# Kernel tuning notes

Hardware: AMD Instinct MI355X
Metric: run time of the kernel (lower is better)

Reference implementation:

```python
import jax, jax.numpy as jnp
import numpy as np

LOG2 = 0.6931471805599453
GAMMA = 10.0
NUM_KERNELS = 301
N_LAYERS = 3


def ssp(v):
    # ShiftedSoftplus: softplus(x) - log(2)
    return jax.nn.softplus(v) - jnp.asarray(LOG2, v.dtype)


def setup_inputs() -> dict:
    key = jax.random.key(0)
    ks = jax.random.split(key, 20)
    N, F, K, L, V = 512, 128, NUM_KERNELS, N_LAYERS, 100
    s = 0.05
    return {
        "x": jax.random.randint(ks[0], (N,), 0, V),
        "r": jax.random.uniform(ks[1], (N, 3), dtype=jnp.float32) * 10.0,
        "emb": jax.random.normal(ks[2], (V, F), dtype=jnp.float32),
        "aw_W": jax.random.normal(ks[3], (L, F, F), dtype=jnp.float32) * s,
        "aw_b": jax.random.normal(ks[4], (L, F), dtype=jnp.float32) * s,
        "cf_W1": jax.random.normal(ks[5], (L, K, F), dtype=jnp.float32) * s,
        "cf_b1": jax.random.normal(ks[6], (L, F), dtype=jnp.float32) * s,
        "cf_W2": jax.random.normal(ks[7], (L, F, F), dtype=jnp.float32) * s,
        "cf_b2": jax.random.normal(ks[8], (L, F), dtype=jnp.float32) * s,
        "n_W1": jax.random.normal(ks[9], (L, F, F), dtype=jnp.float32) * s,
        "n_b1": jax.random.normal(ks[10], (L, F), dtype=jnp.float32) * s,
        "n_W2": jax.random.normal(ks[11], (L, F, F), dtype=jnp.float32) * s,
        "n_b2": jax.random.normal(ks[12], (L, F), dtype=jnp.float32) * s,
        "out_W1": jax.random.normal(ks[13], (F, 32), dtype=jnp.float32) * s,
        "out_b1": jax.random.normal(ks[14], (32,), dtype=jnp.float32) * s,
        "out_W2": jax.random.normal(ks[15], (32, 1), dtype=jnp.float32) * s,
        "out_b2": jax.random.normal(ks[16], (1,), dtype=jnp.float32) * s,
    }


def reference(x, r, emb, aw_W, aw_b, cf_W1, cf_b1, cf_W2, cf_b2,
              n_W1, n_b1, n_W2, n_b2, out_W1, out_b1, out_W2, out_b2):
    centers = jnp.linspace(0.0, 30.0, NUM_KERNELS, dtype=r.dtype)  # [K]
    # pairwise distances (torch.cdist, p=2) with safe sqrt at the diagonal
    diff = r[:, None, :] - r[None, :, :]                 # [N,N,3]
    d2 = jnp.sum(diff * diff, axis=-1)                   # [N,N]
    mask = d2 > 0
    d = jnp.where(mask, jnp.sqrt(jnp.where(mask, d2, 1.0)), 0.0)

    h = emb[x]                                           # [N,F]
    for l in range(N_LAYERS):
        o = h @ aw_W[l] + aw_b[l]                        # atom-wise linear
        # Gaussian RBF expansion: [N,N,K]
        e = jnp.exp(-GAMMA * jnp.square(d[..., None] - centers))
        # filter-generating MLP: [N,N,F]
        w = ssp(e @ cf_W1[l] + cf_b1[l])
        w = ssp(w @ cf_W2[l] + cf_b2[l])
        # continuous-filter conv: o[i,k] = sum_j x[j,k] * w[i,j,k]
        c = jnp.einsum('jk,ijk->ik', o, w)
        c = ssp(c @ n_W1[l] + n_b1[l]) @ n_W2[l] + n_b2[l]
        h = h + c
    out = ssp(h @ out_W1 + out_b1) @ out_W2 + out_b2     # [N,1]
    # AdaptiveAvgPool1d(1) on a 2D [N,1] tensor is identity over L=1
    return out.reshape(-1)
```

## Files before the change

### kernel.cpp

```cpp
#include <hip/hip_runtime.h>
#include <hip/hip_fp16.h>
#include <math.h>

#define N_ATOMS 512
#define F_DIM   128
#define K_RBF   301
#define NLAYER  3
#define GAMMA_C 10.0f
#define LOG2_C  0.6931471805599453f

#define TAB_H     0.01f
#define TAB_INVH  100.0f
#define TAB_ROWS  1768
#define RPB       8
#define ROW_BYTES 512

__device__ __forceinline__ float ssp(float x) {
    float ax = fabsf(x);
    return fmaxf(x, 0.0f) + log1pf(expf(-ax)) - LOG2_C;
}
__device__ __forceinline__ __half2 u2h2(unsigned u) {
    union { unsigned u; __half2 h; } c; c.u = u; return c.h;
}
__device__ __forceinline__ unsigned h22u(__half2 h) {
    union { unsigned u; __half2 h; } c; c.h = h; return c.u;
}

__global__ void prep_kernel(const int* __restrict__ x, const float* __restrict__ r,
                            const float* __restrict__ emb,
                            const float* __restrict__ aw_W, const float* __restrict__ aw_b,
                            uint2* __restrict__ dpk, float* __restrict__ h,
                            unsigned* __restrict__ opk) {
    int i = blockIdx.x;
    int t = threadIdx.x;
    __shared__ float hs[F_DIM];
    __shared__ float os[F_DIM];
    float rx = r[i * 3 + 0], ry = r[i * 3 + 1], rz = r[i * 3 + 2];
    if (t < F_DIM) {
        float hv = emb[x[i] * F_DIM + t];
        h[i * F_DIM + t] = hv;
        hs[t] = hv;
    }
    for (int j = t; j < N_ATOMS; j += 256) {
        float dx = rx - r[j * 3 + 0];
        float dy = ry - r[j * 3 + 1];
        float dz = rz - r[j * 3 + 2];
        float d  = sqrtf(dx * dx + dy * dy + dz * dz);
        float xb = d * TAB_INVH;
        int   b  = ::min((int)xb, TAB_ROWS - 2);
        float fr = xb - (float)b;
        __half fh = __float2half(fr);
        dpk[i * N_ATOMS + j] = make_uint2((unsigned)b * ROW_BYTES,
                                          h22u(__halves2half2(fh, fh)));
    }
    __syncthreads();
    if (t < F_DIM) {
        float acc = aw_b[t];
        for (int g = 0; g < F_DIM; ++g) acc = fmaf(hs[g], aw_W[g * F_DIM + t], acc);
        os[t] = acc;
    }
    __syncthreads();
    if (t < F_DIM / 2)
        opk[i * 64 + t] = h22u(__halves2half2(__float2half(os[2 * t]),
                                              __float2half(os[2 * t + 1])));
}

__global__ void build_tables(const float* __restrict__ cf_W1, const float* __restrict__ cf_b1,
                             const float* __restrict__ cf_W2, const float* __restrict__ cf_b2,
                             uint2* __restrict__ ptab) {
    int row0 = blockIdx.x * RPB;
    int l    = blockIdx.y;
    int f    = threadIdx.x;

    float dlo = row0 * TAB_H;
    float dhi = (row0 + RPB) * TAB_H;
    int k0 = ::max(0, (int)ceilf((dlo - 1.45f) * 10.0f));
    int k1 = ::min(K_RBF - 1, (int)floorf((dhi + 1.45f) * 10.0f));
    int kw = k1 - k0 + 1;

    __shared__ float e_s[RPB + 1][34];
    __shared__ float w1_s[F_DIM][12];
    __shared__ float outs[RPB + 1][F_DIM];

    for (int idx = f; idx < (RPB + 1) * kw; idx += F_DIM) {
        int rr = idx / kw, kk = idx % kw;
        float dv = (row0 + rr) * TAB_H;
        float tt = dv - 0.1f * (float)(k0 + kk);
        e_s[rr][kk] = expf(-GAMMA_C * tt * tt);
    }
    __syncthreads();

    const float* W1 = cf_W1 + l * K_RBF * F_DIM;
    float b1v = cf_b1[l * F_DIM + f];
    float acc[RPB + 1];
#pragma unroll
    for (int rr = 0; rr <= RPB; ++rr) acc[rr] = b1v;
    for (int kk = 0; kk < kw; ++kk) {
        float w1v = W1[(k0 + kk) * F_DIM + f];
#pragma unroll
        for (int rr = 0; rr <= RPB; ++rr) acc[rr] = fmaf(e_s[rr][kk], w1v, acc[rr]);
    }
#pragma unroll
    for (int rr = 0; rr <= RPB; ++rr) w1_s[f][rr] = ssp(acc[rr]);
    __syncthreads();

    const float* W2 = cf_W2 + l * F_DIM * F_DIM;
    float b2v = cf_b2[l * F_DIM + f];
    float acc2[RPB + 1];
#pragma unroll
    for (int rr = 0; rr <= RPB; ++rr) acc2[rr] = b2v;
    for (int g = 0; g < F_DIM; ++g) {
        float w2v = W2[g * F_DIM + f];
        float4 wa = *(const float4*)&w1_s[g][0];
        float4 wb = *(const float4*)&w1_s[g][4];
        float  wc = w1_s[g][8];
        acc2[0] = fmaf(wa.x, w2v, acc2[0]);
        acc2[1] = fmaf(wa.y, w2v, acc2[1]);
        acc2[2] = fmaf(wa.z, w2v, acc2[2]);
        acc2[3] = fmaf(wa.w, w2v, acc2[3]);
        acc2[4] = fmaf(wb.x, w2v, acc2[4]);
        acc2[5] = fmaf(wb.y, w2v, acc2[5]);
        acc2[6] = fmaf(wb.z, w2v, acc2[6]);
        acc2[7] = fmaf(wb.w, w2v, acc2[7]);
        acc2[8] = fmaf(wc,   w2v, acc2[8]);
    }
#pragma unroll
    for (int rr = 0; rr <= RPB; ++rr) outs[rr][f] = ssp(acc2[rr]);
    __syncthreads();

    int p = f & 63;
    int rbase = (f >> 6) * (RPB / 2);
#pragma unroll
    for (int q = 0; q < RPB / 2; ++q) {
        int rr = rbase + q;
        float t00 = outs[rr][2 * p],     t01 = outs[rr][2 * p + 1];
        float n00 = outs[rr + 1][2 * p], n01 = outs[rr + 1][2 * p + 1];
        uint2 v = make_uint2(
            h22u(__halves2half2(__float2half(t00), __float2half(t01))),
            h22u(__halves2half2(__float2half(n00 - t00), __float2half(n01 - t01))));
        ptab[((size_t)l * TAB_ROWS + row0 + rr) * 64 + p] = v;
    }
}

__global__ void __launch_bounds__(512)
conv_kernel(const uint2* __restrict__ dpk, const unsigned* __restrict__ opk,
            const uint2* __restrict__ ptab, float* __restrict__ c, int l) {
    int i  = blockIdx.x;
    int t  = threadIdx.x;
    int p  = t & 63;
    int jc = t >> 6;

    __shared__ uint2  ds[N_ATOMS];
    __shared__ float2 red[8][64];

    ds[t] = dpk[i * N_ATOMS + t];
    __syncthreads();

    const char* T = (const char*)(ptab + (size_t)l * TAB_ROWS * 64) + p * 8;
    float2 acc = make_float2(0.0f, 0.0f);
    int j = jc * 64;
#pragma unroll 4
    for (int jj = 0; jj < 64; ++jj, ++j) {
        uint2 e = ds[j];
        __half2 fr2 = u2h2(e.y);
        uint2 tv = *(const uint2*)(T + e.x);
        __half2 w2 = __hfma2(fr2, u2h2(tv.y), u2h2(tv.x));
        __half2 oh = u2h2(opk[j * 64 + p]);
        acc.x = fmaf(__half2float(__low2half(w2)),  __half2float(__low2half(oh)),  acc.x);
        acc.y = fmaf(__half2float(__high2half(w2)), __half2float(__high2half(oh)), acc.y);
    }
    red[jc][p] = acc;
    __syncthreads();
    if (jc == 0) {
        float2 s = red[0][p];
#pragma unroll
        for (int q = 1; q < 8; ++q) { s.x += red[q][p].x; s.y += red[q][p].y; }
        *(float2*)&c[i * F_DIM + 2 * p] = s;
    }
}

__global__ void node_fused(const float* __restrict__ c, const float* __restrict__ n_W1,
                           const float* __restrict__ n_b1, const float* __restrict__ n_W2,
                           const float* __restrict__ n_b2, float* __restrict__ h,
                           const float* __restrict__ aw_W, const float* __restrict__ aw_b,
                           unsigned* __restrict__ opk,
                           const float* __restrict__ oW1, const float* __restrict__ ob1,
                           const float* __restrict__ oW2, const float* __restrict__ ob2,
                           float* __restrict__ out, int l) {
    int i = blockIdx.x, f = threadIdx.x;
    __shared__ float cs[F_DIM];
    __shared__ float t1s[F_DIM];
    __shared__ float hs[F_DIM];
    cs[f] = c[i * F_DIM + f];
    __syncthreads();
    const float* W1 = n_W1 + l * F_DIM * F_DIM;
    float a = n_b1[l * F_DIM + f];
    for (int g = 0; g < F_DIM; ++g) a = fmaf(cs[g], W1[g * F_DIM + f], a);
    t1s[f] = ssp(a);
    __syncthreads();
    const float* W2 = n_W2 + l * F_DIM * F_DIM;
    float a2 = n_b2[l * F_DIM + f];
    for (int g = 0; g < F_DIM; ++g) a2 = fmaf(t1s[g], W2[g * F_DIM + f], a2);
    float hv = h[i * F_DIM + f] + a2;
    h[i * F_DIM + f] = hv;
    hs[f] = hv;
    __syncthreads();

    if (l < NLAYER - 1) {
        const float* W = aw_W + (l + 1) * F_DIM * F_DIM;
        float acc = aw_b[(l + 1) * F_DIM + f];
        for (int g = 0; g < F_DIM; ++g) acc = fmaf(hs[g], W[g * F_DIM + f], acc);
        t1s[f] = acc;
        __syncthreads();
        if (f < F_DIM / 2)
            opk[i * 64 + f] = h22u(__halves2half2(__float2half(t1s[2 * f]),
                                                  __float2half(t1s[2 * f + 1])));
    } else {
        float val = 0.0f;
        if (f < 32) {
            float ah = ob1[f];
            for (int g = 0; g < F_DIM; ++g) ah = fmaf(hs[g], oW1[g * 32 + f], ah);
            val = ssp(ah) * oW2[f];
        }
#pragma unroll
        for (int off = 16; off > 0; off >>= 1) val += __shfl_xor(val, off, 64);
        if (f == 0) out[i] = val + ob2[0];
    }
}

extern "C" void kernel_launch(void* const* d_in, const int* in_sizes, int n_in,
                              void* d_out, int out_size, void* d_ws, size_t ws_size,
                              hipStream_t stream) {
    const int*   x     = (const int*)  d_in[0];
    const float* r     = (const float*)d_in[1];
    const float* emb   = (const float*)d_in[2];
    const float* aw_W  = (const float*)d_in[3];
    const float* aw_b  = (const float*)d_in[4];
    const float* cf_W1 = (const float*)d_in[5];
    const float* cf_b1 = (const float*)d_in[6];
    const float* cf_W2 = (const float*)d_in[7];
    const float* cf_b2 = (const float*)d_in[8];
    const float* n_W1  = (const float*)d_in[9];
    const float* n_b1  = (const float*)d_in[10];
    const float* n_W2  = (const float*)d_in[11];
    const float* n_b2  = (const float*)d_in[12];
    const float* oW1   = (const float*)d_in[13];
    const float* ob1   = (const float*)d_in[14];
    const float* oW2   = (const float*)d_in[15];
    const float* ob2   = (const float*)d_in[16];
    float* out = (float*)d_out;

    char* ws = (char*)d_ws;
    uint2*    dpk  = (uint2*)ws;    ws += (size_t)N_ATOMS * N_ATOMS * 8;
    float*    h    = (float*)ws;    ws += (size_t)N_ATOMS * F_DIM * 4;
    unsigned* opk  = (unsigned*)ws; ws += (size_t)N_ATOMS * (F_DIM / 2) * 4;
    float*    c    = (float*)ws;    ws += (size_t)N_ATOMS * F_DIM * 4;
    uint2*    ptab = (uint2*)ws;

    prep_kernel<<<N_ATOMS, 256, 0, stream>>>(x, r, emb, aw_W, aw_b, dpk, h, opk);
    build_tables<<<dim3(TAB_ROWS / RPB, NLAYER), 128, 0, stream>>>(cf_W1, cf_b1, cf_W2, cf_b2, ptab);
    for (int l = 0; l < NLAYER; ++l) {
        conv_kernel<<<N_ATOMS, 512, 0, stream>>>(dpk, opk, ptab, c, l);
        node_fused<<<N_ATOMS, 128, 0, stream>>>(c, n_W1, n_b1, n_W2, n_b2, h,
                                                aw_W, aw_b, opk, oW1, ob1, oW2, ob2, out, l);
    }
}
```

Before: 175.2 us.

## Fuse prep with table build and conv with node MLP, ping-pong opk buffers

Merges the prep and table-building kernels into one launch, where extra blocks each handle two table tasks, and fuses the per-layer conv kernel with the node MLP kernel. The conv result now stays in shared memory instead of going through a global buffer. Double-buffered opk arrays avoid read/write races across blocks. This cuts the launch count from 8 to 4 and removes the global round-trip of c. In exchange, the node MLP runs on only 128 of 512 threads in the fused block and holds the larger block's resources longer.

```diff
diff --git a/kernel.cpp b/kernel.cpp
--- a/kernel.cpp
+++ b/kernel.cpp
@@ -13,6 +13,9 @@
 #define TAB_INVH  100.0f
 #define TAB_ROWS  1768
 #define RPB       8
+#define NGROUPS   (TAB_ROWS / RPB)
+#define NTASKS    (NGROUPS * NLAYER)
+#define NBBLK     ((NTASKS + 1) / 2)
 #define ROW_BYTES 512
 
 __device__ __forceinline__ float ssp(float x) {
@@ -26,51 +29,61 @@
     union { unsigned u; __half2 h; } c; c.h = h; return c.u;
 }
 
-__global__ void prep_kernel(const int* __restrict__ x, const float* __restrict__ r,
-                            const float* __restrict__ emb,
-                            const float* __restrict__ aw_W, const float* __restrict__ aw_b,
-                            uint2* __restrict__ dpk, float* __restrict__ h,
-                            unsigned* __restrict__ opk) {
-    int i = blockIdx.x;
-    int t = threadIdx.x;
+__global__ void __launch_bounds__(256)
+prep_build(const int* __restrict__ x, const float* __restrict__ r,
+           const float* __restrict__ emb,
+           const float* __restrict__ aw_W, const float* __restrict__ aw_b,
+           const float* __restrict__ cf_W1, const float* __restrict__ cf_b1,
+           const float* __restrict__ cf_W2, const float* __restrict__ cf_b2,
+           uint2* __restrict__ dpk, float* __restrict__ h,
+           unsigned* __restrict__ opk, uint2* __restrict__ ptab) {
     __shared__ float hs[F_DIM];
     __shared__ float os[F_DIM];
-    float rx = r[i * 3 + 0], ry = r[i * 3 + 1], rz = r[i * 3 + 2];
-    if (t < F_DIM) {
-        float hv = emb[x[i] * F_DIM + t];
-        h[i * F_DIM + t] = hv;
-        hs[t] = hv;
-    }
-    for (int j = t; j < N_ATOMS; j += 256) {
-        float dx = rx - r[j * 3 + 0];
-        float dy = ry - r[j * 3 + 1];
-        float dz = rz - r[j * 3 + 2];
-        float d  = sqrtf(dx * dx + dy * dy + dz * dz);
-        float xb = d * TAB_INVH;
-        int   b  = ::min((int)xb, TAB_ROWS - 2);
-        float fr = xb - (float)b;
-        __half fh = __float2half(fr);
-        dpk[i * N_ATOMS + j] = make_uint2((unsigned)b * ROW_BYTES,
-                                          h22u(__halves2half2(fh, fh)));
-    }
-    __syncthreads();
-    if (t < F_DIM) {
-        float acc = aw_b[t];
-        for (int g = 0; g < F_DIM; ++g) acc = fmaf(hs[g], aw_W[g * F_DIM + t], acc);
-        os[t] = acc;
-    }
-    __syncthreads();
-    if (t < F_DIM / 2)
-        opk[i * 64 + t] = h22u(__halves2half2(__float2half(os[2 * t]),
-                                              __float2half(os[2 * t + 1])));
-}
-
-__global__ void build_tables(const float* __restrict__ cf_W1, const float* __restrict__ cf_b1,
-                             const float* __restrict__ cf_W2, const float* __restrict__ cf_b2,
-                             uint2* __restrict__ ptab) {
-    int row0 = blockIdx.x * RPB;
-    int l    = blockIdx.y;
-    int f    = threadIdx.x;
+    __shared__ float e_s[2][RPB + 1][34];
+    __shared__ float w1_s[2][F_DIM][12];
+    __shared__ float outs[2][RPB + 1][F_DIM];
+
+    if (blockIdx.x < N_ATOMS) {
+        int i = blockIdx.x;
+        int t = threadIdx.x;
+        float rx = r[i * 3 + 0], ry = r[i * 3 + 1], rz = r[i * 3 + 2];
+        if (t < F_DIM) {
+            float hv = emb[x[i] * F_DIM + t];
+            h[i * F_DIM + t] = hv;
+            hs[t] = hv;
+        }
+        for (int j = t; j < N_ATOMS; j += 256) {
+            float dx = rx - r[j * 3 + 0];
+            float dy = ry - r[j * 3 + 1];
+            float dz = rz - r[j * 3 + 2];
+            float d  = sqrtf(dx * dx + dy * dy + dz * dz);
+            float xb = d * TAB_INVH;
+            int   b  = ::min((int)xb, TAB_ROWS - 2);
+            float fr = xb - (float)b;
+            __half fh = __float2half(fr);
+            dpk[i * N_ATOMS + j] = make_uint2((unsigned)b * ROW_BYTES,
+                                              h22u(__halves2half2(fh, fh)));
+        }
+        __syncthreads();
+        if (t < F_DIM) {
+            float acc = aw_b[t];
+            for (int g = 0; g < F_DIM; ++g) acc = fmaf(hs[g], aw_W[g * F_DIM + t], acc);
+            os[t] = acc;
+        }
+        __syncthreads();
+        if (t < F_DIM / 2)
+            opk[i * 64 + t] = h22u(__halves2half2(__float2half(os[2 * t]),
+                                                  __float2half(os[2 * t + 1])));
+        return;
+    }
+
+    int u = threadIdx.x >> 7;
+    int f = threadIdx.x & 127;
+    int task = (blockIdx.x - N_ATOMS) * 2 + u;
+    bool valid = task < NTASKS;
+    task = ::min(task, NTASKS - 1);
+    int l    = task / NGROUPS;
+    int row0 = (task % NGROUPS) * RPB;
 
     float dlo = row0 * TAB_H;
     float dhi = (row0 + RPB) * TAB_H;
@@ -78,15 +91,11 @@
     int k1 = ::min(K_RBF - 1, (int)floorf((dhi + 1.45f) * 10.0f));
     int kw = k1 - k0 + 1;
 
-    __shared__ float e_s[RPB + 1][34];
-    __shared__ float w1_s[F_DIM][12];
-    __shared__ float outs[RPB + 1][F_DIM];
-
     for (int idx = f; idx < (RPB + 1) * kw; idx += F_DIM) {
         int rr = idx / kw, kk = idx % kw;
         float dv = (row0 + rr) * TAB_H;
         float tt = dv - 0.1f * (float)(k0 + kk);
-        e_s[rr][kk] = expf(-GAMMA_C * tt * tt);
+        e_s[u][rr][kk] = expf(-GAMMA_C * tt * tt);
     }
     __syncthreads();
 
@@ -98,10 +107,10 @@
     for (int kk = 0; kk < kw; ++kk) {
         float w1v = W1[(k0 + kk) * F_DIM + f];
 #pragma unroll
-        for (int rr = 0; rr <= RPB; ++rr) acc[rr] = fmaf(e_s[rr][kk], w1v, acc[rr]);
-    }
-#pragma unroll
-    for (int rr = 0; rr <= RPB; ++rr) w1_s[f][rr] = ssp(acc[rr]);
+        for (int rr = 0; rr <= RPB; ++rr) acc[rr] = fmaf(e_s[u][rr][kk], w1v, acc[rr]);
+    }
+#pragma unroll
+    for (int rr = 0; rr <= RPB; ++rr) w1_s[u][f][rr] = ssp(acc[rr]);
     __syncthreads();
 
     const float* W2 = cf_W2 + l * F_DIM * F_DIM;
@@ -111,9 +120,9 @@
     for (int rr = 0; rr <= RPB; ++rr) acc2[rr] = b2v;
     for (int g = 0; g < F_DIM; ++g) {
         float w2v = W2[g * F_DIM + f];
-        float4 wa = *(const float4*)&w1_s[g][0];
-        float4 wb = *(const float4*)&w1_s[g][4];
-        float  wc = w1_s[g][8];
+        float4 wa = *(const float4*)&w1_s[u][g][0];
+        float4 wb = *(const float4*)&w1_s[u][g][4];
+        float  wc = w1_s[u][g][8];
         acc2[0] = fmaf(wa.x, w2v, acc2[0]);
         acc2[1] = fmaf(wa.y, w2v, acc2[1]);
         acc2[2] = fmaf(wa.z, w2v, acc2[2]);
@@ -125,26 +134,36 @@
         acc2[8] = fmaf(wc,   w2v, acc2[8]);
     }
 #pragma unroll
-    for (int rr = 0; rr <= RPB; ++rr) outs[rr][f] = ssp(acc2[rr]);
-    __syncthreads();
-
-    int p = f & 63;
-    int rbase = (f >> 6) * (RPB / 2);
-#pragma unroll
-    for (int q = 0; q < RPB / 2; ++q) {
-        int rr = rbase + q;
-        float t00 = outs[rr][2 * p],     t01 = outs[rr][2 * p + 1];
-        float n00 = outs[rr + 1][2 * p], n01 = outs[rr + 1][2 * p + 1];
-        uint2 v = make_uint2(
-            h22u(__halves2half2(__float2half(t00), __float2half(t01))),
-            h22u(__halves2half2(__float2half(n00 - t00), __float2half(n01 - t01))));
-        ptab[((size_t)l * TAB_ROWS + row0 + rr) * 64 + p] = v;
+    for (int rr = 0; rr <= RPB; ++rr) outs[u][rr][f] = ssp(acc2[rr]);
+    __syncthreads();
+
+    if (valid) {
+        int p = f & 63;
+        int rbase = (f >> 6) * (RPB / 2);
+#pragma unroll
+        for (int q = 0; q < RPB / 2; ++q) {
+            int rr = rbase + q;
+            float t00 = outs[u][rr][2 * p],     t01 = outs[u][rr][2 * p + 1];
+            float n00 = outs[u][rr + 1][2 * p], n01 = outs[u][rr + 1][2 * p + 1];
+            uint2 v = make_uint2(
+                h22u(__halves2half2(__float2half(t00), __float2half(t01))),
+                h22u(__halves2half2(__float2half(n00 - t00), __float2half(n01 - t01))));
+            ptab[((size_t)l * TAB_ROWS + row0 + rr) * 64 + p] = v;
+        }
     }
 }
 
 __global__ void __launch_bounds__(512)
-conv_kernel(const uint2* __restrict__ dpk, const unsigned* __restrict__ opk,
-            const uint2* __restrict__ ptab, float* __restrict__ c, int l) {
+convnode_kernel(const uint2* __restrict__ dpk, const unsigned* __restrict__ opk_in,
+                const uint2* __restrict__ ptab,
+                const float* __restrict__ n_W1, const float* __restrict__ n_b1,
+                const float* __restrict__ n_W2, const float* __restrict__ n_b2,
+                float* __restrict__ h,
+                const float* __restrict__ aw_W, const float* __restrict__ aw_b,
+                unsigned* __restrict__ opk_out,
+                const float* __restrict__ oW1, const float* __restrict__ ob1,
+                const float* __restrict__ oW2, const float* __restrict__ ob2,
+                float* __restrict__ out, int l) {
     int i  = blockIdx.x;
     int t  = threadIdx.x;
     int p  = t & 63;
@@ -152,8 +171,12 @@
 
     __shared__ uint2  ds[N_ATOMS];
     __shared__ float2 red[8][64];
+    __shared__ float  cs[F_DIM];
+    __shared__ float  t1s[F_DIM];
+    __shared__ float  hs[F_DIM];
 
     ds[t] = dpk[i * N_ATOMS + t];
+    if (t < F_DIM) hs[t] = h[i * F_DIM + t];
     __syncthreads();
 
     const char* T = (const char*)(ptab + (size_t)l * TAB_ROWS * 64) + p * 8;
@@ -162,10 +185,9 @@
 #pragma unroll 4
     for (int jj = 0; jj < 64; ++jj, ++j) {
         uint2 e = ds[j];
-        __half2 fr2 = u2h2(e.y);
         uint2 tv = *(const uint2*)(T + e.x);
-        __half2 w2 = __hfma2(fr2, u2h2(tv.y), u2h2(tv.x));
-        __half2 oh = u2h2(opk[j * 64 + p]);
+        __half2 w2 = __hfma2(u2h2(e.y), u2h2(tv.y), u2h2(tv.x));
+        __half2 oh = u2h2(opk_in[j * 64 + p]);
         acc.x = fmaf(__half2float(__low2half(w2)),  __half2float(__low2half(oh)),  acc.x);
         acc.y = fmaf(__half2float(__high2half(w2)), __half2float(__high2half(oh)), acc.y);
     }
@@ -175,56 +197,48 @@
         float2 s = red[0][p];
 #pragma unroll
         for (int q = 1; q < 8; ++q) { s.x += red[q][p].x; s.y += red[q][p].y; }
-        *(float2*)&c[i * F_DIM + 2 * p] = s;
-    }
-}
-
-__global__ void node_fused(const float* __restrict__ c, const float* __restrict__ n_W1,
-                           const float* __restrict__ n_b1, const float* __restrict__ n_W2,
-                           const float* __restrict__ n_b2, float* __restrict__ h,
-                           const float* __restrict__ aw_W, const float* __restrict__ aw_b,
-                           unsigned* __restrict__ opk,
-                           const float* __restrict__ oW1, const float* __restrict__ ob1,
-                           const float* __restrict__ oW2, const float* __restrict__ ob2,
-                           float* __restrict__ out, int l) {
-    int i = blockIdx.x, f = threadIdx.x;
-    __shared__ float cs[F_DIM];
-    __shared__ float t1s[F_DIM];
-    __shared__ float hs[F_DIM];
-    cs[f] = c[i * F_DIM + f];
-    __syncthreads();
-    const float* W1 = n_W1 + l * F_DIM * F_DIM;
-    float a = n_b1[l * F_DIM + f];
-    for (int g = 0; g < F_DIM; ++g) a = fmaf(cs[g], W1[g * F_DIM + f], a);
-    t1s[f] = ssp(a);
-    __syncthreads();
-    const float* W2 = n_W2 + l * F_DIM * F_DIM;
-    float a2 = n_b2[l * F_DIM + f];
-    for (int g = 0; g < F_DIM; ++g) a2 = fmaf(t1s[g], W2[g * F_DIM + f], a2);
-    float hv = h[i * F_DIM + f] + a2;
-    h[i * F_DIM + f] = hv;
-    hs[f] = hv;
+        *(float2*)&cs[2 * p] = s;
+    }
+    __syncthreads();
+
+    if (t < F_DIM) {
+        const float* W1 = n_W1 + l * F_DIM * F_DIM;
+        float a = n_b1[l * F_DIM + t];
+        for (int g = 0; g < F_DIM; ++g) a = fmaf(cs[g], W1[g * F_DIM + t], a);
+        t1s[t] = ssp(a);
+    }
+    __syncthreads();
+    if (t < F_DIM) {
+        const float* W2 = n_W2 + l * F_DIM * F_DIM;
+        float a2 = n_b2[l * F_DIM + t];
+        for (int g = 0; g < F_DIM; ++g) a2 = fmaf(t1s[g], W2[g * F_DIM + t], a2);
+        float hv = hs[t] + a2;
+        h[i * F_DIM + t] = hv;
+        hs[t] = hv;
+    }
     __syncthreads();
 
     if (l < NLAYER - 1) {
-        const float* W = aw_W + (l + 1) * F_DIM * F_DIM;
-        float acc = aw_b[(l + 1) * F_DIM + f];
-        for (int g = 0; g < F_DIM; ++g) acc = fmaf(hs[g], W[g * F_DIM + f], acc);
-        t1s[f] = acc;
+        if (t < F_DIM) {
+            const float* W = aw_W + (l + 1) * F_DIM * F_DIM;
+            float a = aw_b[(l + 1) * F_DIM + t];
+            for (int g = 0; g < F_DIM; ++g) a = fmaf(hs[g], W[g * F_DIM + t], a);
+            t1s[t] = a;
+        }
         __syncthreads();
-        if (f < F_DIM / 2)
-            opk[i * 64 + f] = h22u(__halves2half2(__float2half(t1s[2 * f]),
-                                                  __float2half(t1s[2 * f + 1])));
+        if (t < F_DIM / 2)
+            opk_out[i * 64 + t] = h22u(__halves2half2(__float2half(t1s[2 * t]),
+                                                      __float2half(t1s[2 * t + 1])));
     } else {
         float val = 0.0f;
-        if (f < 32) {
-            float ah = ob1[f];
-            for (int g = 0; g < F_DIM; ++g) ah = fmaf(hs[g], oW1[g * 32 + f], ah);
-            val = ssp(ah) * oW2[f];
+        if (t < 32) {
+            float ah = ob1[t];
+            for (int g = 0; g < F_DIM; ++g) ah = fmaf(hs[g], oW1[g * 32 + t], ah);
+            val = ssp(ah) * oW2[t];
         }
 #pragma unroll
         for (int off = 16; off > 0; off >>= 1) val += __shfl_xor(val, off, 64);
-        if (f == 0) out[i] = val + ob2[0];
+        if (t == 0) out[i] = val + ob2[0];
     }
 }
 
@@ -253,15 +267,17 @@
     char* ws = (char*)d_ws;
     uint2*    dpk  = (uint2*)ws;    ws += (size_t)N_ATOMS * N_ATOMS * 8;
     float*    h    = (float*)ws;    ws += (size_t)N_ATOMS * F_DIM * 4;
-    unsigned* opk  = (unsigned*)ws; ws += (size_t)N_ATOMS * (F_DIM / 2) * 4;
-    float*    c    = (float*)ws;    ws += (size_t)N_ATOMS * F_DIM * 4;
+    unsigned* opkA = (unsigned*)ws; ws += (size_t)N_ATOMS * (F_DIM / 2) * 4;
+    unsigned* opkB = (unsigned*)ws; ws += (size_t)N_ATOMS * (F_DIM / 2) * 4;
     uint2*    ptab = (uint2*)ws;
 
-    prep_kernel<<<N_ATOMS, 256, 0, stream>>>(x, r, emb, aw_W, aw_b, dpk, h, opk);
-    build_tables<<<dim3(TAB_ROWS / RPB, NLAYER), 128, 0, stream>>>(cf_W1, cf_b1, cf_W2, cf_b2, ptab);
+    prep_build<<<N_ATOMS + NBBLK, 256, 0, stream>>>(
+        x, r, emb, aw_W, aw_b, cf_W1, cf_b1, cf_W2, cf_b2, dpk, h, opkA, ptab);
     for (int l = 0; l < NLAYER; ++l) {
-        conv_kernel<<<N_ATOMS, 512, 0, stream>>>(dpk, opk, ptab, c, l);
-        node_fused<<<N_ATOMS, 128, 0, stream>>>(c, n_W1, n_b1, n_W2, n_b2, h,
-                                                aw_W, aw_b, opk, oW1, ob1, oW2, ob2, out, l);
-    }
-}
+        unsigned* oin  = (l & 1) ? opkB : opkA;
+        unsigned* oout = (l & 1) ? opkA : opkB;
+        convnode_kernel<<<N_ATOMS, 512, 0, stream>>>(
+            dpk, oin, ptab, n_W1, n_b1, n_W2, n_b2, h,
+            aw_W, aw_b, oout, oW1, ob1, oW2, ob2, out, l);
+    }
+}
```

After: 169.0 us. 3.5% less time.
